# Kernel tuning notes

Hardware: AMD Instinct MI355X
Metric: run time of the kernel (lower is better)

The kernel has to match this reference:

```python
import jax, jax.numpy as jnp
import numpy as np
from jax import lax

NEGINF = -100000.0
START_IDX = 0  # y_codebook['__START__']
TAGSET = 16


def setup_inputs() -> dict:
    key = jax.random.key(0)
    ks = jax.random.split(key, 8)
    D, H, K, T = 1024, 1024, TAGSET, 8192
    seq = jax.random.normal(ks[0], (1, T, D), dtype=jnp.float32)
    # PyTorch-layout LSTM params: gates ordered (i, f, g, o)
    s = 1.0 / np.sqrt(H)
    W_ih = jax.random.uniform(ks[1], (4 * H, D), jnp.float32, -s, s)
    W_hh = jax.random.uniform(ks[2], (4 * H, H), jnp.float32, -s, s)
    b_ih = jax.random.uniform(ks[3], (4 * H,), jnp.float32, -s, s)
    b_hh = jax.random.uniform(ks[4], (4 * H,), jnp.float32, -s, s)
    W_tag = jax.random.uniform(ks[5], (K, H), jnp.float32, -s, s)
    b_tag = jax.random.uniform(ks[6], (K,), jnp.float32, -s, s)
    trans = jax.random.normal(ks[7], (K, K), dtype=jnp.float32)
    trans = trans.at[:, START_IDX].set(NEGINF)  # nothing transitions INTO start
    return {"seq": seq, "W_ih": W_ih, "W_hh": W_hh, "b_ih": b_ih,
            "b_hh": b_hh, "W_tag": W_tag, "b_tag": b_tag, "trans": trans}


def _lstm(x, W_ih, W_hh, b_ih, b_hh):
    # x: (T, D) -> hidden states (T, H); PyTorch gate order i,f,g,o
    H = W_hh.shape[1]
    x_gates = x @ W_ih.T + (b_ih + b_hh)  # (T, 4H) precomputed input part

    def step(carry, gx):
        h, c = carry
        g = gx + h @ W_hh.T
        i, f, gg, o = jnp.split(g, 4)
        i, f, o = jax.nn.sigmoid(i), jax.nn.sigmoid(f), jax.nn.sigmoid(o)
        c = f * c + i * jnp.tanh(gg)
        h = o * jnp.tanh(c)
        return (h, c), h

    init = (jnp.zeros((H,), x.dtype), jnp.zeros((H,), x.dtype))
    _, hs = lax.scan(step, init, x_gates)
    return hs  # (T, H)


def reference(seq, W_ih, W_hh, b_ih, b_hh, W_tag, b_tag, trans):
    # --- compute_potential (batch=1) ---
    x = seq[0]                                  # (T, D)
    rnnout = _lstm(x, W_ih, W_hh, b_ih, b_hh)    # (T, H)
    feat = rnnout @ W_tag.T + b_tag              # (T, K) unary potentials

    # --- compute_forward_vec: alpha recursion in log-semiring ---
    # feat_score[t, i, j] = feat[t, j] + trans[i, j]
    feat_score = feat[:, None, :] + trans[None, :, :]  # (T, K, K)
    K = trans.shape[0]
    alpha0 = jnp.full((K,), NEGINF, dtype=feat.dtype).at[START_IDX].set(0.0)

    def step(a, fs):
        a_new = jax.nn.logsumexp(a[:, None] + fs, axis=0)  # (K,)
        return a_new, a_new

    a_T, rows = lax.scan(step, alpha0, feat_score)
    alpha = jnp.concatenate([alpha0[None, :], rows], axis=0)  # (T+1, K)
    Z = jax.nn.logsumexp(a_T)  # log partition (no stop state)
    return Z, alpha
```

## Files before the change

kernel.cpp:

```cpp
#include <hip/hip_runtime.h>
#include <hip/hip_bf16.h>
#include <math.h>

#define T_LEN   8192
#define D_IN    1024
#define H_DIM   1024
#define G4      4096
#define K_TAG   16
#define NWG     128
#define NPAIR   512
#define NC      128
#define CLEN    64
#define NEGINF_V (-100000.0f)

__global__ void k_init(const float* __restrict__ b_ih, const float* __restrict__ b_hh,
                       float* __restrict__ bsum, float* __restrict__ h0,
                       unsigned long long* __restrict__ htag) {
  int tid = blockIdx.x * 256 + threadIdx.x;
  if (tid < G4) bsum[tid] = b_ih[tid] + b_hh[tid];
  if (tid < H_DIM) h0[tid] = 0.f;
  if (tid < 2 * NPAIR) htag[tid] = 0ULL;
}

__global__ __launch_bounds__(256) void k_gemm_xg(
    const float* __restrict__ A,
    const float* __restrict__ B,
    const float* __restrict__ bsum,
    __hip_bfloat16* __restrict__ xg)
{
  __shared__ __align__(16) float As[16][132];
  __shared__ __align__(16) float Bs[16][132];
  const int tid = threadIdx.x;
  const int n0 = blockIdx.x * 128;
  const int m0 = blockIdx.y * 128;
  const int ty = tid >> 4, tx = tid & 15;
  float acc[8][8] = {};

  for (int k0 = 0; k0 < D_IN; k0 += 16) {
#pragma unroll
    for (int p0 = 0; p0 < 2; ++p0) {
      int p = tid + p0 * 256;
      int row = p >> 2;
      int c4 = (p & 3) * 4;
      float4 va = *(const float4*)&A[(size_t)(m0 + row) * D_IN + k0 + c4];
      As[c4 + 0][row] = va.x; As[c4 + 1][row] = va.y;
      As[c4 + 2][row] = va.z; As[c4 + 3][row] = va.w;
      float4 vb = *(const float4*)&B[(size_t)(n0 + row) * D_IN + k0 + c4];
      Bs[c4 + 0][row] = vb.x; Bs[c4 + 1][row] = vb.y;
      Bs[c4 + 2][row] = vb.z; Bs[c4 + 3][row] = vb.w;
    }
    __syncthreads();
#pragma unroll
    for (int k = 0; k < 16; ++k) {
      float4 a0 = *(const float4*)&As[k][ty * 8];
      float4 a1 = *(const float4*)&As[k][ty * 8 + 4];
      float4 b0 = *(const float4*)&Bs[k][tx * 8];
      float4 b1 = *(const float4*)&Bs[k][tx * 8 + 4];
      float av[8] = {a0.x, a0.y, a0.z, a0.w, a1.x, a1.y, a1.z, a1.w};
      float bv[8] = {b0.x, b0.y, b0.z, b0.w, b1.x, b1.y, b1.z, b1.w};
#pragma unroll
      for (int i = 0; i < 8; ++i)
#pragma unroll
        for (int j = 0; j < 8; ++j)
          acc[i][j] = fmaf(av[i], bv[j], acc[i][j]);
    }
    __syncthreads();
  }

#pragma unroll
  for (int i = 0; i < 8; ++i) {
    size_t m = (size_t)(m0 + ty * 8 + i);
    union { __hip_bfloat16 h[8]; uint4 v; } pk;
#pragma unroll
    for (int j = 0; j < 8; ++j)
      pk.h[j] = __float2bfloat16(acc[i][j] + bsum[n0 + tx * 8 + j]);
    *(uint4*)&xg[m * G4 + n0 + tx * 8] = pk.v;
  }
}

__global__ __launch_bounds__(256) void k_lstm(
    const float* __restrict__ W_hh,
    const __hip_bfloat16* __restrict__ xg,
    float* __restrict__ h_all,
    unsigned long long* __restrict__ htag)
{
  __shared__ __align__(16) float h_lds[H_DIM];
  __shared__ unsigned hx[4];

  const int tid = threadIdx.x;
  const int w = blockIdx.x;
  const int lane = tid & 63;
  const int v = tid >> 6;
  const int rl8 = lane >> 3;
  const int sub = lane & 7;
  const int g = rl8 >> 1, b = rl8 & 1;
  const int j = 2 * v + b;
  const int grow = g * H_DIM + w * 8 + j;

  float4 w4[32];
#pragma unroll
  for (int k = 0; k < 32; ++k)
    w4[k] = *(const float4*)&W_hh[(size_t)grow * H_DIM + sub * 4 + 32 * k];

  float c_reg = 0.f;

  for (int t = 1; t <= T_LEN; ++t) {
    float xgv = __bfloat162float(xg[(size_t)(t - 1) * G4 + grow]);

    if (v == 0) {
      unsigned long long* hb = htag + (((t - 1) & 1) << 9);
      const unsigned tgt = (unsigned)(t - 1);
      unsigned long long x0, x1, x2, x3, x4, x5, x6, x7;
      for (;;) {
        x0 = __hip_atomic_load(hb + lane,       __ATOMIC_RELAXED, __HIP_MEMORY_SCOPE_AGENT);
        x1 = __hip_atomic_load(hb + lane + 64,  __ATOMIC_RELAXED, __HIP_MEMORY_SCOPE_AGENT);
        x2 = __hip_atomic_load(hb + lane + 128, __ATOMIC_RELAXED, __HIP_MEMORY_SCOPE_AGENT);
        x3 = __hip_atomic_load(hb + lane + 192, __ATOMIC_RELAXED, __HIP_MEMORY_SCOPE_AGENT);
        x4 = __hip_atomic_load(hb + lane + 256, __ATOMIC_RELAXED, __HIP_MEMORY_SCOPE_AGENT);
        x5 = __hip_atomic_load(hb + lane + 320, __ATOMIC_RELAXED, __HIP_MEMORY_SCOPE_AGENT);
        x6 = __hip_atomic_load(hb + lane + 384, __ATOMIC_RELAXED, __HIP_MEMORY_SCOPE_AGENT);
        x7 = __hip_atomic_load(hb + lane + 448, __ATOMIC_RELAXED, __HIP_MEMORY_SCOPE_AGENT);
        unsigned mn = min(min(min((unsigned)(x0 >> 32), (unsigned)(x1 >> 32)),
                              min((unsigned)(x2 >> 32), (unsigned)(x3 >> 32))),
                          min(min((unsigned)(x4 >> 32), (unsigned)(x5 >> 32)),
                              min((unsigned)(x6 >> 32), (unsigned)(x7 >> 32))));
        if (mn >= tgt) break;
        __builtin_amdgcn_s_sleep(2);
      }
      unsigned long long xs[8] = {x0, x1, x2, x3, x4, x5, x6, x7};
#pragma unroll
      for (int i = 0; i < 8; ++i) {
        unsigned lo = (unsigned)xs[i];
        unsigned short s0 = (unsigned short)lo;
        unsigned short s1 = (unsigned short)(lo >> 16);
        float2 p;
        p.x = __bfloat162float(*(const __hip_bfloat16*)&s0);
        p.y = __bfloat162float(*(const __hip_bfloat16*)&s1);
        ((float2*)h_lds)[lane + 64 * i] = p;
      }
    }
    __syncthreads();

    const float4* h4 = (const float4*)h_lds;
    float acc = 0.f;
#pragma unroll
    for (int k = 0; k < 32; ++k) {
      float4 hv = h4[sub + 8 * k];
      acc = fmaf(w4[k].x, hv.x, acc);
      acc = fmaf(w4[k].y, hv.y, acc);
      acc = fmaf(w4[k].z, hv.z, acc);
      acc = fmaf(w4[k].w, hv.w, acc);
    }
    acc += __shfl_xor(acc, 1);
    acc += __shfl_xor(acc, 2);
    acc += __shfl_xor(acc, 4);
    acc += xgv;

    const int bl = lane & 8;
    float gi = __shfl(acc, bl);
    float gf = __shfl(acc, bl | 16);
    float gg = __shfl(acc, bl | 32);
    float go = __shfl(acc, bl | 48);

    float si = 1.f / (1.f + expf(-gi));
    float sf = 1.f / (1.f + expf(-gf));
    float so = 1.f / (1.f + expf(-go));
    c_reg = sf * c_reg + si * tanhf(gg);
    float h = so * tanhf(c_reg);
    float h_other = __shfl(h, lane ^ 8);

    if (lane == 0) {
      __hip_bfloat16 hb0 = __float2bfloat16(h);
      __hip_bfloat16 hb1 = __float2bfloat16(h_other);
      hx[v] = (unsigned)*(unsigned short*)&hb0 |
              ((unsigned)*(unsigned short*)&hb1 << 16);
    }
    if ((lane & 55) == 0) {
      h_all[(size_t)t * H_DIM + w * 8 + j] = h;
    }
    __syncthreads();

    if (v == 0 && lane < 4) {
      unsigned long long pk = ((unsigned long long)(unsigned)t << 32) |
                              (unsigned long long)hx[lane];
      __hip_atomic_store(htag + ((t & 1) << 9) + w * 4 + lane, pk,
                         __ATOMIC_RELAXED, __HIP_MEMORY_SCOPE_AGENT);
    }
  }
}

__device__ __forceinline__ float lse16(float v) {
  float m = v;
  m = fmaxf(m, __shfl_xor(m, 1));
  m = fmaxf(m, __shfl_xor(m, 2));
  m = fmaxf(m, __shfl_xor(m, 4));
  m = fmaxf(m, __shfl_xor(m, 8));
  float e = expf(v - m);
  e += __shfl_xor(e, 1);
  e += __shfl_xor(e, 2);
  e += __shfl_xor(e, 4);
  e += __shfl_xor(e, 8);
  return m + logf(e);
}

__global__ __launch_bounds__(256) void k_chunk(
    const float* __restrict__ h_all,
    const float* __restrict__ W_tag, const float* __restrict__ b_tag,
    const float* __restrict__ trans,
    float* __restrict__ featbuf,
    float* __restrict__ Pbuf)
{
  __shared__ float trs[16][17];
  __shared__ float featc[CLEN][16];
  __shared__ __align__(16) float hrow[H_DIM];
  __shared__ float red[16][17];
  __shared__ float Pa[16][17], Pb[16][17];

  const int tid = threadIdx.x;
  const int c = blockIdx.x;
  trs[tid >> 4][tid & 15] = trans[tid];

  const int jj = tid & 15, part = tid >> 4;
  for (int u = 0; u < CLEN; ++u) {
    int s = c * CLEN + 1 + u;
    ((float4*)hrow)[tid] = ((const float4*)(h_all + (size_t)s * H_DIM))[tid];
    __syncthreads();
    const float* wt = W_tag + (size_t)jj * H_DIM + part * 64;
    const float* hp = hrow + part * 64;
    float4 a4 = {0.f, 0.f, 0.f, 0.f};
#pragma unroll
    for (int k2 = 0; k2 < 64; k2 += 4) {
      float4 hv = *(const float4*)(hp + k2);
      float4 wv = *(const float4*)(wt + k2);
      a4.x = fmaf(hv.x, wv.x, a4.x);
      a4.y = fmaf(hv.y, wv.y, a4.y);
      a4.z = fmaf(hv.z, wv.z, a4.z);
      a4.w = fmaf(hv.w, wv.w, a4.w);
    }
    red[jj][part] = (a4.x + a4.y) + (a4.z + a4.w);
    __syncthreads();
    if (tid < 16) {
      float ssum = b_tag[tid];
#pragma unroll
      for (int pp = 0; pp < 16; ++pp) ssum += red[tid][pp];
      featc[u][tid] = ssum;
      featbuf[(size_t)s * K_TAG + tid] = ssum;
    }
    __syncthreads();
  }

  const int i = tid >> 4, j = tid & 15;
  Pa[i][j] = trs[i][j] + featc[0][j];
  __syncthreads();
  float* Pr = &Pa[0][0];
  float* Pw = &Pb[0][0];
  for (int u = 1; u < CLEN; ++u) {
    float fj = featc[u][j];
    float m = -3.0e38f;
#pragma unroll
    for (int k = 0; k < 16; ++k) m = fmaxf(m, Pr[i * 17 + k] + trs[k][j]);
    float e = 0.f;
#pragma unroll
    for (int k = 0; k < 16; ++k) e += expf(Pr[i * 17 + k] + trs[k][j] - m);
    Pw[i * 17 + j] = m + fj + logf(e);
    __syncthreads();
    float* tsw = Pr; Pr = Pw; Pw = tsw;
  }
  Pbuf[(size_t)c * 256 + i * 16 + j] = Pr[i * 17 + j];
}

__global__ __launch_bounds__(256) void k_scan(
    const float* __restrict__ Pbuf,
    float* __restrict__ bbuf,
    float* __restrict__ out)
{
  __shared__ float Pl[16][17];
  __shared__ float bcur[16], bnew[16];
  const int tid = threadIdx.x;
  const int i = tid & 15, j = tid >> 4;
  if (tid < 16) {
    float a0 = (tid == 0) ? 0.f : NEGINF_V;
    bcur[tid] = a0;
    bbuf[tid] = a0;
    out[1 + tid] = a0;
  }
  __syncthreads();
  for (int c = 0; c < NC; ++c) {
    Pl[tid >> 4][tid & 15] = Pbuf[(size_t)c * 256 + tid];
    __syncthreads();
    float r_ = lse16(bcur[i] + Pl[i][j]);
    if (i == 0) bnew[j] = r_;
    __syncthreads();
    if (tid < 16) {
      bcur[tid] = bnew[tid];
      bbuf[(size_t)(c + 1) * K_TAG + tid] = bnew[tid];
    }
    __syncthreads();
  }
  if (tid < 16) {
    float z = lse16(bcur[tid]);
    if (tid == 0) out[0] = z;
  }
}

__global__ __launch_bounds__(256) void k_alpha(
    const float* __restrict__ featbuf, const float* __restrict__ trans,
    const float* __restrict__ bbuf, float* __restrict__ out)
{
  __shared__ float trs[16][17];
  __shared__ float acur[16], anew[16];
  const int tid = threadIdx.x;
  const int c = blockIdx.x;
  trs[tid >> 4][tid & 15] = trans[tid];
  if (tid < 16) acur[tid] = bbuf[(size_t)c * K_TAG + tid];
  __syncthreads();
  const int i = tid & 15, j = tid >> 4;
  for (int u = 0; u < CLEN; ++u) {
    int s = c * CLEN + 1 + u;
    float v = acur[i] + trs[i][j] + featbuf[(size_t)s * K_TAG + j];
    float r_ = lse16(v);
    if (i == 0) anew[j] = r_;
    __syncthreads();
    if (tid < 16) {
      acur[tid] = anew[tid];
      out[1 + (size_t)s * K_TAG + tid] = anew[tid];
    }
    __syncthreads();
  }
}

extern "C" void kernel_launch(void* const* d_in, const int* in_sizes, int n_in,
                              void* d_out, int out_size, void* d_ws, size_t ws_size,
                              hipStream_t stream) {
  (void)in_sizes; (void)n_in; (void)out_size; (void)ws_size;
  const float* seq   = (const float*)d_in[0];
  const float* W_ih  = (const float*)d_in[1];
  const float* W_hh  = (const float*)d_in[2];
  const float* b_ih  = (const float*)d_in[3];
  const float* b_hh  = (const float*)d_in[4];
  const float* W_tag = (const float*)d_in[5];
  const float* b_tag = (const float*)d_in[6];
  const float* trans = (const float*)d_in[7];
  float* out = (float*)d_out;

  char* base = (char*)d_ws;
  size_t off = 0;
  auto take = [&](size_t nbytes) -> void* {
    void* p = base + off;
    off += (nbytes + 255) & ~(size_t)255;
    return p;
  };
  __hip_bfloat16* xg = (__hip_bfloat16*)take((size_t)T_LEN * G4 * sizeof(__hip_bfloat16));
  float* h_all   = (float*)take((size_t)(T_LEN + 1) * H_DIM * sizeof(float));
  float* featbuf = (float*)take((size_t)(T_LEN + 1) * K_TAG * sizeof(float));
  float* Pbuf    = (float*)take((size_t)NC * 256 * sizeof(float));
  float* bbuf    = (float*)take((size_t)(NC + 1) * K_TAG * sizeof(float));
  float* bsum    = (float*)take((size_t)G4 * sizeof(float));
  unsigned long long* htag = (unsigned long long*)take((size_t)2 * NPAIR * sizeof(unsigned long long));

  k_init<<<16, 256, 0, stream>>>(b_ih, b_hh, bsum, h_all, htag);
  k_gemm_xg<<<dim3(G4 / 128, T_LEN / 128), 256, 0, stream>>>(seq, W_ih, bsum, xg);
  k_lstm<<<NWG, 256, 0, stream>>>(W_hh, xg, h_all, htag);
  k_chunk<<<NC, 256, 0, stream>>>(h_all, W_tag, b_tag, trans, featbuf, Pbuf);
  k_scan<<<1, 256, 0, stream>>>(Pbuf, bbuf, out);
  k_alpha<<<NC, 256, 0, stream>>>(featbuf, trans, bbuf, out);
}
```

Baseline: 21.14 ms.

## Stream h chunks into LDS with per-chunk ready flags and fast gate math

The barrier after the global spin-wait is replaced by per-chunk readiness. The polling wave copies each 128-element chunk of h into LDS as soon as all its tags are current and sets an LDS flag. The compute waves spin on those flags and start the dot product on ready chunks, so the matvec overlaps arrival of the slower producers. Sigmoid and tanh also move to fast __expf/__fdividef versions, which shortens the serial per-step tail but slightly lowers accuracy; LDS spin-waiting across waves risks contention and depends on memory-ordering assumptions.

```diff
diff --git a/kernel.cpp b/kernel.cpp
--- a/kernel.cpp
+++ b/kernel.cpp
@@ -13,6 +13,14 @@
 #define CLEN    64
 #define NEGINF_V (-100000.0f)
 
+__device__ __forceinline__ float fsig(float x) {
+  return __fdividef(1.f, 1.f + __expf(-x));
+}
+__device__ __forceinline__ float ftanh(float x) {
+  float e = __expf(fminf(fmaxf(2.f * x, -88.f), 88.f));
+  return __fdividef(e - 1.f, e + 1.f);
+}
+
 __global__ void k_init(const float* __restrict__ b_ih, const float* __restrict__ b_hh,
                        float* __restrict__ bsum, float* __restrict__ h0,
                        unsigned long long* __restrict__ htag) {
@@ -85,6 +93,7 @@
     unsigned long long* __restrict__ htag)
 {
   __shared__ __align__(16) float h_lds[H_DIM];
+  __shared__ unsigned grdy[8];
   __shared__ unsigned hx[4];
 
   const int tid = threadIdx.x;
@@ -102,6 +111,9 @@
   for (int k = 0; k < 32; ++k)
     w4[k] = *(const float4*)&W_hh[(size_t)grow * H_DIM + sub * 4 + 32 * k];
 
+  if (tid < 8) grdy[tid] = 0;
+  __syncthreads();
+
   float c_reg = 0.f;
 
   for (int t = 1; t <= T_LEN; ++t) {
@@ -110,46 +122,52 @@
     if (v == 0) {
       unsigned long long* hb = htag + (((t - 1) & 1) << 9);
       const unsigned tgt = (unsigned)(t - 1);
-      unsigned long long x0, x1, x2, x3, x4, x5, x6, x7;
-      for (;;) {
-        x0 = __hip_atomic_load(hb + lane,       __ATOMIC_RELAXED, __HIP_MEMORY_SCOPE_AGENT);
-        x1 = __hip_atomic_load(hb + lane + 64,  __ATOMIC_RELAXED, __HIP_MEMORY_SCOPE_AGENT);
-        x2 = __hip_atomic_load(hb + lane + 128, __ATOMIC_RELAXED, __HIP_MEMORY_SCOPE_AGENT);
-        x3 = __hip_atomic_load(hb + lane + 192, __ATOMIC_RELAXED, __HIP_MEMORY_SCOPE_AGENT);
-        x4 = __hip_atomic_load(hb + lane + 256, __ATOMIC_RELAXED, __HIP_MEMORY_SCOPE_AGENT);
-        x5 = __hip_atomic_load(hb + lane + 320, __ATOMIC_RELAXED, __HIP_MEMORY_SCOPE_AGENT);
-        x6 = __hip_atomic_load(hb + lane + 384, __ATOMIC_RELAXED, __HIP_MEMORY_SCOPE_AGENT);
-        x7 = __hip_atomic_load(hb + lane + 448, __ATOMIC_RELAXED, __HIP_MEMORY_SCOPE_AGENT);
-        unsigned mn = min(min(min((unsigned)(x0 >> 32), (unsigned)(x1 >> 32)),
-                              min((unsigned)(x2 >> 32), (unsigned)(x3 >> 32))),
-                          min(min((unsigned)(x4 >> 32), (unsigned)(x5 >> 32)),
-                              min((unsigned)(x6 >> 32), (unsigned)(x7 >> 32))));
-        if (mn >= tgt) break;
-        __builtin_amdgcn_s_sleep(2);
+      unsigned done = 0;
+      while (done != 0xffu) {
+        unsigned long long x[8];
+#pragma unroll
+        for (int i = 0; i < 8; ++i)
+          if (!((done >> i) & 1))
+            x[i] = __hip_atomic_load(hb + lane + 64 * i,
+                                     __ATOMIC_RELAXED, __HIP_MEMORY_SCOPE_AGENT);
+        bool any = false;
+#pragma unroll
+        for (int i = 0; i < 8; ++i) {
+          if (!((done >> i) & 1)) {
+            if (__all((int)((unsigned)(x[i] >> 32) >= tgt))) {
+              unsigned lo = (unsigned)x[i];
+              unsigned short s0 = (unsigned short)lo;
+              unsigned short s1 = (unsigned short)(lo >> 16);
+              float2 pr;
+              pr.x = __bfloat162float(*(const __hip_bfloat16*)&s0);
+              pr.y = __bfloat162float(*(const __hip_bfloat16*)&s1);
+              ((float2*)h_lds)[lane + 64 * i] = pr;
+              __threadfence_block();
+              if (lane == 0) grdy[i] = (unsigned)t;
+              done |= 1u << i;
+              any = true;
+            }
+          }
+        }
+        if (!any) __builtin_amdgcn_s_sleep(1);
       }
-      unsigned long long xs[8] = {x0, x1, x2, x3, x4, x5, x6, x7};
-#pragma unroll
-      for (int i = 0; i < 8; ++i) {
-        unsigned lo = (unsigned)xs[i];
-        unsigned short s0 = (unsigned short)lo;
-        unsigned short s1 = (unsigned short)(lo >> 16);
-        float2 p;
-        p.x = __bfloat162float(*(const __hip_bfloat16*)&s0);
-        p.y = __bfloat162float(*(const __hip_bfloat16*)&s1);
-        ((float2*)h_lds)[lane + 64 * i] = p;
+    }
+
+    float acc = 0.f;
+    const float4* h4 = (const float4*)h_lds;
+#pragma unroll
+    for (int g2 = 0; g2 < 8; ++g2) {
+      while (*(volatile unsigned*)&grdy[g2] != (unsigned)t) {}
+      asm volatile("" ::: "memory");
+#pragma unroll
+      for (int kk = 0; kk < 4; ++kk) {
+        const int k = 4 * g2 + kk;
+        float4 hv = h4[sub + 8 * k];
+        acc = fmaf(w4[k].x, hv.x, acc);
+        acc = fmaf(w4[k].y, hv.y, acc);
+        acc = fmaf(w4[k].z, hv.z, acc);
+        acc = fmaf(w4[k].w, hv.w, acc);
       }
-    }
-    __syncthreads();
-
-    const float4* h4 = (const float4*)h_lds;
-    float acc = 0.f;
-#pragma unroll
-    for (int k = 0; k < 32; ++k) {
-      float4 hv = h4[sub + 8 * k];
-      acc = fmaf(w4[k].x, hv.x, acc);
-      acc = fmaf(w4[k].y, hv.y, acc);
-      acc = fmaf(w4[k].z, hv.z, acc);
-      acc = fmaf(w4[k].w, hv.w, acc);
     }
     acc += __shfl_xor(acc, 1);
     acc += __shfl_xor(acc, 2);
@@ -162,11 +180,11 @@
     float gg = __shfl(acc, bl | 32);
     float go = __shfl(acc, bl | 48);
 
-    float si = 1.f / (1.f + expf(-gi));
-    float sf = 1.f / (1.f + expf(-gf));
-    float so = 1.f / (1.f + expf(-go));
-    c_reg = sf * c_reg + si * tanhf(gg);
-    float h = so * tanhf(c_reg);
+    float si = fsig(gi);
+    float sf = fsig(gf);
+    float so = fsig(go);
+    c_reg = sf * c_reg + si * ftanh(gg);
+    float h = so * ftanh(c_reg);
     float h_other = __shfl(h, lane ^ 8);
 
     if (lane == 0) {
```

New measurement: 26.80 ms. +26.8%, slower.
